# Kernel optimization log

Measured on AMD Instinct MI355X. Metric: run time of the kernel, lower is better.

The kernel has to match this reference:

```python
import jax, jax.numpy as jnp
import numpy as np

N_NODES = 100000
N_EDGES = 3200000
N_GRAPHS = 1000
HID = 64
L = 4  # num_unit


def setup_inputs() -> dict:
    key = jax.random.key(0)
    ks = jax.random.split(key, 16)
    x = jax.random.normal(ks[0], (N_NODES, 4), dtype=jnp.float32)
    edge_index = jax.random.randint(ks[1], (2, N_EDGES), 0, N_NODES, dtype=jnp.int64)
    edge_attr = jax.random.uniform(ks[2], (N_EDGES,), dtype=jnp.float32)
    batch = jnp.sort(jax.random.randint(ks[3], (N_NODES,), 0, N_GRAPHS, dtype=jnp.int64))
    s = 1.0 / np.sqrt(HID)
    inp = {
        'x': x, 'edge_index': edge_index, 'edge_attr': edge_attr, 'batch': batch,
        'emb_w': jax.random.normal(ks[4], (4, HID), jnp.float32) * 0.5,
        'emb_b': jnp.zeros((HID,), jnp.float32),
        'conv_w1': jax.random.normal(ks[5], (L, HID, HID), jnp.float32) * s,
        'conv_b1': jnp.zeros((L, HID), jnp.float32),
        'conv_w2': jax.random.normal(ks[6], (L, HID, HID), jnp.float32) * s,
        'conv_w3': jax.random.normal(ks[7], (L, HID, HID), jnp.float32) * s,
        'conv_b3': jnp.zeros((L, HID), jnp.float32),
        'lin1_w': jax.random.normal(ks[8], (HID, HID), jnp.float32) * s,
        'lin1_b': jnp.zeros((HID,), jnp.float32),
        'lin2_w': jax.random.normal(ks[9], (HID, 3), jnp.float32) * s,
        'lin2_b': jnp.zeros((3,), jnp.float32),
    }
    return inp


def _forward(x, edge_index, edge_attr, batch,
             emb_w, emb_b, conv_w1, conv_b1, conv_w2, conv_w3, conv_b3,
             lin1_w, lin1_b, lin2_w, lin2_b):
    src, dst = edge_index[0], edge_index[1]
    ew = edge_attr[:, None]  # [E,1]
    h = x @ emb_w + emb_b  # node_emb; dropout omitted (eval mode)
    for l in range(conv_w1.shape[0]):
        # LEConv: out_i = sum_{j->i} w_ji * (lin1(x_j) - lin2(x_i)) + lin3(x_i)
        a = h @ conv_w1[l] + conv_b1[l]
        b = h @ conv_w2[l]  # no bias
        msg = (a[src] - b[dst]) * ew  # [E, HID]
        agg = jax.ops.segment_sum(msg, dst, num_segments=h.shape[0])
        h = jax.nn.relu(agg + h @ conv_w3[l] + conv_b3[l])
    # global mean pool over graphs
    sums = jax.ops.segment_sum(h, batch, num_segments=N_GRAPHS)
    cnt = jax.ops.segment_sum(jnp.ones((h.shape[0],), h.dtype), batch, num_segments=N_GRAPHS)
    graph_x = sums / jnp.maximum(cnt, 1.0)[:, None]
    pred = jax.nn.relu(graph_x @ lin1_w + lin1_b) @ lin2_w + lin2_b
    return pred


def reference(x, edge_index, edge_attr, batch, emb_w, emb_b,
              conv_w1, conv_b1, conv_w2, conv_w3, conv_b3,
              lin1_w, lin1_b, lin2_w, lin2_b):
    return _forward(x, edge_index, edge_attr, batch, emb_w, emb_b,
                    conv_w1, conv_b1, conv_w2, conv_w3, conv_b3,
                    lin1_w, lin1_b, lin2_w, lin2_b)
```

## Files before the change

### kernel.cpp

```cpp
#include <hip/hip_runtime.h>

#define N_NODES 100000
#define N_EDGES 3200000
#define N_GRAPHS 1000
#define NLAYER 4
#define NB 782
#define BBITS 7
#define CAP 4608
#define EPB 2048
#define GSC 1563

typedef __attribute__((ext_vector_type(8))) short bf16x8;
typedef __attribute__((ext_vector_type(4))) float f32x4;

static __device__ __forceinline__ unsigned f2bf(float f) {
  unsigned u = __float_as_uint(f);
  return (u + 0x7fffu + ((u >> 16) & 1u)) >> 16;
}
static __device__ __forceinline__ float bf2f_lo(unsigned u) {
  return __uint_as_float(u << 16);
}
static __device__ __forceinline__ float bf2f_hi(unsigned u) {
  return __uint_as_float(u & 0xffff0000u);
}

__global__ __launch_bounds__(256) void embed_kernel(
    const float* __restrict__ x, const float* __restrict__ emb_w,
    const float* __restrict__ emb_b, unsigned short* __restrict__ h_bf,
    int* __restrict__ gcur)
{
  if (blockIdx.x == 0) {
    for (int i = threadIdx.x; i < NB; i += 256) gcur[i] = i * CAP;
  }
  int t = blockIdx.x * 256 + threadIdx.x;
  if (t >= N_NODES * 64) return;
  int c = t & 63, v = t >> 6;
  float4 xv = ((const float4*)x)[v];
  float acc = emb_b[c];
  acc = fmaf(xv.x, emb_w[0 * 64 + c], acc);
  acc = fmaf(xv.y, emb_w[1 * 64 + c], acc);
  acc = fmaf(xv.z, emb_w[2 * 64 + c], acc);
  acc = fmaf(xv.w, emb_w[3 * 64 + c], acc);
  h_bf[t] = (unsigned short)f2bf(acc);
}

__global__ __launch_bounds__(256) void bscatter5_kernel(
    const int* __restrict__ ei, const float* __restrict__ ea,
    int* __restrict__ gcur, unsigned* __restrict__ tmp_w,
    unsigned char* __restrict__ tmp_d)
{
  __shared__ unsigned hist[NB];
  __shared__ int dif[NB];
  __shared__ unsigned stage_w[EPB];
  __shared__ unsigned char stage_d[EPB];
  __shared__ unsigned short bid[EPB];
  __shared__ int wpart[4];
  int tid = threadIdx.x;
  int base = blockIdx.x * EPB;

  for (int i = tid; i < NB; i += 256) hist[i] = 0;
  __syncthreads();

  int dreg[8];
#pragma unroll
  for (int i = 0; i < 8; ++i) {
    int e = base + i * 256 + tid;
    dreg[i] = -1;
    if (e < N_EDGES) {
      int d = ei[N_EDGES + e];
      dreg[i] = d;
      atomicAdd(&hist[((unsigned)d) >> BBITS], 1u);
    }
  }
  __syncthreads();

  int lane = tid & 63, w = tid >> 6;
  int b0 = tid * 4;
  int c[4];
  int tsum = 0;
#pragma unroll
  for (int k = 0; k < 4; ++k) {
    int b = b0 + k;
    c[k] = (b < NB) ? (int)hist[b] : 0;
    tsum += c[k];
  }
  int s = tsum;
#pragma unroll
  for (int off = 1; off < 64; off <<= 1) {
    int y = __shfl_up(s, off);
    if (lane >= off) s += y;
  }
  if (lane == 63) wpart[w] = s;
  __syncthreads();
  int wo = 0;
  for (int ww = 0; ww < w; ++ww) wo += wpart[ww];
  int excl = wo + (s - tsum);
#pragma unroll
  for (int k = 0; k < 4; ++k) {
    int b = b0 + k;
    if (b < NB) {
      int gb = c[k] ? atomicAdd(&gcur[b], c[k]) : 0;
      dif[b] = gb - excl;
      hist[b] = (unsigned)excl;
      excl += c[k];
    }
  }
  __syncthreads();

#pragma unroll
  for (int i = 0; i < 8; ++i) {
    int e = base + i * 256 + tid;
    int d = dreg[i];
    if (d >= 0) {
      unsigned bkt = ((unsigned)d) >> BBITS;
      unsigned lp = atomicAdd(&hist[bkt], 1u);
      unsigned q15 = (unsigned)(ea[e] * 32768.0f);
      stage_w[lp] = ((unsigned)ei[e]) | (q15 << 17);
      stage_d[lp] = (unsigned char)(d & 127);
      bid[lp] = (unsigned short)bkt;
    }
  }
  __syncthreads();

  int nE = min(EPB, N_EDGES - base);
  for (int i = tid; i < nE; i += 256) {
    int g = dif[bid[i]] + i;
    tmp_w[g] = stage_w[i];
    tmp_d[g] = stage_d[i];
  }
}

__global__ __launch_bounds__(256) void bucket_sort4_kernel(
    const int* __restrict__ gcur, const unsigned* __restrict__ tmp_w,
    const unsigned char* __restrict__ tmp_d,
    unsigned* __restrict__ csr, int* __restrict__ row_off,
    unsigned short* __restrict__ deg16, float* __restrict__ degw)
{
  int j = blockIdx.x;
  int b0 = j * CAP;
  int nE = gcur[j] - b0;
  __shared__ unsigned hist[128];
  __shared__ float dws[128];
  __shared__ unsigned cur[128];
  __shared__ int wpart[2];
  __shared__ unsigned short perm[CAP];
  int t = threadIdx.x;
  if (t < 128) { hist[t] = 0; dws[t] = 0.f; }
  __syncthreads();
  for (int i = t; i < nE; i += 256) {
    unsigned d = tmp_d[b0 + i];
    unsigned wrd = tmp_w[b0 + i];
    atomicAdd(&hist[d], 1u);
    atomicAdd(&dws[d], (float)(wrd >> 17) * (1.0f / 32768.0f));
  }
  __syncthreads();
  int lane = t & 63, w = t >> 6;
  int v = (t < 128) ? (int)hist[t] : 0;
  int s = v;
#pragma unroll
  for (int off = 1; off < 64; off <<= 1) {
    int y = __shfl_up(s, off);
    if (lane >= off) s += y;
  }
  if (t < 128 && lane == 63) wpart[w] = s;
  __syncthreads();
  if (t < 128) {
    int wo = (w == 1) ? wpart[0] : 0;
    int excl = wo + s - v;
    cur[t] = (unsigned)excl;
    int vnode = (j << BBITS) + t;
    if (vnode < N_NODES) {
      row_off[vnode] = b0 + excl;
      deg16[vnode] = (unsigned short)v;
      degw[vnode] = dws[t];
    }
  }
  __syncthreads();

  for (int i = t; i < nE; i += 256) {
    unsigned p = atomicAdd(&cur[tmp_d[b0 + i]], 1u);
    perm[p] = (unsigned short)i;
  }
  __syncthreads();
  for (int q = t; q < nE; q += 256)
    csr[b0 + q] = tmp_w[b0 + (int)perm[q]];
}

__global__ __launch_bounds__(256) void wswz_kernel(
    const float* __restrict__ cw1, const float* __restrict__ cw2,
    const float* __restrict__ cw3, unsigned* __restrict__ wswz)
{
  int l = blockIdx.x;
  const float* w1 = cw1 + l * 4096;
  const float* w2 = cw2 + l * 4096;
  const float* w3 = cw3 + l * 4096;
  unsigned* outp = wswz + l * 6144;
  int tid = threadIdx.x;
  int n = tid & 63;
  int gofs = tid >> 6;
  for (int it = 0; it < 24; ++it) {
    int g = it * 4 + gofs;
    int m = g >> 5;
    int kp = g & 31;
    int k = kp * 2;
    const float* W = (m == 0) ? w2 : (m == 1) ? w3 : w1;
    unsigned lo = f2bf(W[k * 64 + n]);
    unsigned hi = f2bf(W[(k + 1) * 64 + n]);
    int c = k >> 5;
    int kk = k & 31;
    int lane = ((kk >> 3) << 4) | (n & 15);
    int j2 = (kk & 7) >> 1;
    int t = n >> 4;
    outp[(((m * 2 + c) * 4 + t) << 8) | (lane << 2) | j2] = lo | (hi << 16);
  }
}

__global__ __launch_bounds__(256) void matvec3_mfma_kernel(
    const unsigned short* __restrict__ h_bf,
    const unsigned* __restrict__ wz,
    const float* __restrict__ b1, const float* __restrict__ b3,
    const float* __restrict__ degw,
    unsigned short* __restrict__ a_bf, unsigned short* __restrict__ cc_bf)
{
  int gw = (blockIdx.x * 256 + threadIdx.x) >> 6;
  int lane = threadIdx.x & 63;
  int quad = lane >> 4;
  int col = lane & 15;
  int nb = gw * 16;
  if (nb >= N_NODES) return;

  int arow = nb + col;
  if (arow >= N_NODES) arow = N_NODES - 1;
  const bf16x8* ap = (const bf16x8*)(h_bf + (size_t)arow * 64 + quad * 8);
  bf16x8 af0 = ap[0];
  bf16x8 af1 = ap[4];

  float dwr[4];
#pragma unroll
  for (int r = 0; r < 4; ++r) {
    int row = nb + quad * 4 + r;
    dwr[r] = degw[row < N_NODES ? row : 0];
  }

#pragma unroll
  for (int t = 0; t < 4; ++t) {
    const bf16x8* b20 = (const bf16x8*)&wz[((0 * 4 + t) << 8) + lane * 4];
    const bf16x8* b21 = (const bf16x8*)&wz[((1 * 4 + t) << 8) + lane * 4];
    const bf16x8* b30 = (const bf16x8*)&wz[((2 * 4 + t) << 8) + lane * 4];
    const bf16x8* b31 = (const bf16x8*)&wz[((3 * 4 + t) << 8) + lane * 4];
    const bf16x8* b10 = (const bf16x8*)&wz[((4 * 4 + t) << 8) + lane * 4];
    const bf16x8* b11 = (const bf16x8*)&wz[((5 * 4 + t) << 8) + lane * 4];

    f32x4 z = {0.f, 0.f, 0.f, 0.f};
    f32x4 acc2 = __builtin_amdgcn_mfma_f32_16x16x32_bf16(af0, *b20, z, 0, 0, 0);
    acc2 = __builtin_amdgcn_mfma_f32_16x16x32_bf16(af1, *b21, acc2, 0, 0, 0);
    f32x4 cc;
#pragma unroll
    for (int r = 0; r < 4; ++r) cc[r] = -dwr[r] * acc2[r];
    cc = __builtin_amdgcn_mfma_f32_16x16x32_bf16(af0, *b30, cc, 0, 0, 0);
    cc = __builtin_amdgcn_mfma_f32_16x16x32_bf16(af1, *b31, cc, 0, 0, 0);
    float bb3 = b3[t * 16 + col];
#pragma unroll
    for (int r = 0; r < 4; ++r) {
      int row = nb + quad * 4 + r;
      if (row < N_NODES)
        cc_bf[(size_t)row * 64 + t * 16 + col] = (unsigned short)f2bf(cc[r] + bb3);
    }

    float bb1 = b1[t * 16 + col];
    f32x4 a1 = {bb1, bb1, bb1, bb1};
    a1 = __builtin_amdgcn_mfma_f32_16x16x32_bf16(af0, *b10, a1, 0, 0, 0);
    a1 = __builtin_amdgcn_mfma_f32_16x16x32_bf16(af1, *b11, a1, 0, 0, 0);
#pragma unroll
    for (int r = 0; r < 4; ++r) {
      int row = nb + quad * 4 + r;
      if (row < N_NODES)
        a_bf[(size_t)row * 64 + t * 16 + col] = (unsigned short)f2bf(a1[r]);
    }
  }
}

__global__ __launch_bounds__(256) void agg_kernel(
    const uint2* __restrict__ a2, const uint2* __restrict__ cc2,
    const int* __restrict__ row_off, const unsigned short* __restrict__ deg16,
    const unsigned* __restrict__ csr,
    float4* __restrict__ h4, unsigned short* __restrict__ h_bf, int write_h)
{
  int wave = (blockIdx.x * 256 + threadIdx.x) >> 6;
  int lane = threadIdx.x & 63;
  int sg = lane >> 4;
  int li = lane & 15;
  int lsel = (lane & 48) << 2;
  int v = wave * 4 + sg;
  bool valid = v < N_NODES;
  int vc = valid ? v : N_NODES - 1;
  int base = row_off[vc];
  int ecnt = valid ? (int)deg16[vc] : 0;
  int emax = ecnt;
  emax = max(emax, __shfl_xor(emax, 16));
  emax = max(emax, __shfl_xor(emax, 32));

  float4 acc = make_float4(0.f, 0.f, 0.f, 0.f);
  if (valid) {
    uint2 cu = cc2[(size_t)vc * 16 + li];
    acc.x = bf2f_lo(cu.x);
    acc.y = bf2f_hi(cu.x);
    acc.z = bf2f_lo(cu.y);
    acc.w = bf2f_hi(cu.y);
  }
  const uint2* ap = a2 + li;

  int full = emax & ~15;
  int c0 = 0;
  for (; c0 < full; c0 += 16) {
    int idx = c0 + li;
    int er = (idx < ecnt) ? (int)csr[base + idx] : 0;
#pragma unroll
    for (int j = 0; j < 16; ++j) {
      unsigned r = (unsigned)__builtin_amdgcn_ds_bpermute(lsel | (j << 2), er);
      int s = (int)(r & 0x1FFFFu);
      float w = (float)(r >> 17) * (1.0f / 32768.0f);
      uint2 u = ap[(size_t)s * 16];
      acc.x = fmaf(w, bf2f_lo(u.x), acc.x);
      acc.y = fmaf(w, bf2f_hi(u.x), acc.y);
      acc.z = fmaf(w, bf2f_lo(u.y), acc.z);
      acc.w = fmaf(w, bf2f_hi(u.y), acc.w);
    }
  }
  int rem = emax - full;
  if (rem > 0) {
    int idx = c0 + li;
    int er = (idx < ecnt) ? (int)csr[base + idx] : 0;
    for (int j = 0; j < rem; ++j) {
      unsigned r = (unsigned)__builtin_amdgcn_ds_bpermute(lsel | (j << 2), er);
      int s = (int)(r & 0x1FFFFu);
      float w = (float)(r >> 17) * (1.0f / 32768.0f);
      uint2 u = ap[(size_t)s * 16];
      acc.x = fmaf(w, bf2f_lo(u.x), acc.x);
      acc.y = fmaf(w, bf2f_hi(u.x), acc.y);
      acc.z = fmaf(w, bf2f_lo(u.y), acc.z);
      acc.w = fmaf(w, bf2f_hi(u.y), acc.w);
    }
  }
  if (valid) {
    acc.x = fmaxf(acc.x, 0.f);
    acc.y = fmaxf(acc.y, 0.f);
    acc.z = fmaxf(acc.z, 0.f);
    acc.w = fmaxf(acc.w, 0.f);
    if (write_h) h4[(size_t)v * 16 + li] = acc;
    uint2 p;
    p.x = f2bf(acc.x) | (f2bf(acc.y) << 16);
    p.y = f2bf(acc.z) | (f2bf(acc.w) << 16);
    ((uint2*)h_bf)[(size_t)v * 16 + li] = p;
  }
}

__global__ __launch_bounds__(256) void head_kernel(
    const float* __restrict__ h, const int* __restrict__ batch,
    const float* __restrict__ l1w, const float* __restrict__ l1b,
    const float* __restrict__ l2w, const float* __restrict__ l2b,
    float* __restrict__ out)
{
  int g = (blockIdx.x * 256 + threadIdx.x) >> 6;
  int lane = threadIdx.x & 63;
  if (g >= N_GRAPHS) return;
  int lo = 0, hi = N_NODES;
  while (lo < hi) { int mid = (lo + hi) >> 1; if (batch[mid] < g) lo = mid + 1; else hi = mid; }
  int start = lo;
  hi = N_NODES;
  while (lo < hi) { int mid = (lo + hi) >> 1; if (batch[mid] < g + 1) lo = mid + 1; else hi = mid; }
  int end = lo;

  float sum = 0.f;
  for (int v = start; v < end; ++v) sum += h[(size_t)v * 64 + lane];
  float cntf = (float)(end - start);
  float gx = sum / fmaxf(cntf, 1.f);

  float acc = l1b[lane];
  for (int k = 0; k < 64; ++k) {
    float gxk = __shfl(gx, k);
    acc = fmaf(gxk, l1w[k * 64 + lane], acc);
  }
  float t = fmaxf(acc, 0.f);
  float p0 = t * l2w[lane * 3 + 0];
  float p1 = t * l2w[lane * 3 + 1];
  float p2 = t * l2w[lane * 3 + 2];
  for (int off = 32; off > 0; off >>= 1) {
    p0 += __shfl_down(p0, off);
    p1 += __shfl_down(p1, off);
    p2 += __shfl_down(p2, off);
  }
  if (lane == 0) {
    out[g * 3 + 0] = p0 + l2b[0];
    out[g * 3 + 1] = p1 + l2b[1];
    out[g * 3 + 2] = p2 + l2b[2];
  }
}

extern "C" void kernel_launch(void* const* d_in, const int* in_sizes, int n_in,
                              void* d_out, int out_size, void* d_ws, size_t ws_size,
                              hipStream_t stream)
{
  (void)in_sizes; (void)n_in; (void)out_size; (void)ws_size;
  const float* x     = (const float*)d_in[0];
  const int*   ei    = (const int*)d_in[1];
  const float* ea    = (const float*)d_in[2];
  const int*   batch = (const int*)d_in[3];
  const float* emb_w = (const float*)d_in[4];
  const float* emb_b = (const float*)d_in[5];
  const float* cw1   = (const float*)d_in[6];
  const float* cb1   = (const float*)d_in[7];
  const float* cw2   = (const float*)d_in[8];
  const float* cw3   = (const float*)d_in[9];
  const float* cb3   = (const float*)d_in[10];
  const float* l1w   = (const float*)d_in[11];
  const float* l1b   = (const float*)d_in[12];
  const float* l2w   = (const float*)d_in[13];
  const float* l2b   = (const float*)d_in[14];
  float* out = (float*)d_out;

  char* wsb = (char*)d_ws;
  size_t off = 0;
  auto alloc = [&](size_t bytes) {
    char* p = wsb + off;
    off = (off + bytes + 255) & ~(size_t)255;
    return p;
  };
  float* h       = (float*)alloc(sizeof(float) * (size_t)N_NODES * 64);
  unsigned short* h_bf = (unsigned short*)alloc(sizeof(short) * (size_t)N_NODES * 64);
  unsigned short* a_bf = (unsigned short*)alloc(sizeof(short) * (size_t)N_NODES * 64);
  unsigned short* cc_bf = (unsigned short*)alloc(sizeof(short) * (size_t)N_NODES * 64);
  unsigned* csr  = (unsigned*)alloc(sizeof(unsigned) * (size_t)NB * CAP);
  int*   row_off = (int*)alloc(sizeof(int) * N_NODES);
  unsigned short* deg16 = (unsigned short*)alloc(sizeof(short) * N_NODES);
  float* degw    = (float*)alloc(sizeof(float) * N_NODES);
  int*   gcur    = (int*)alloc(sizeof(int) * NB);
  unsigned* wswz = (unsigned*)alloc(sizeof(unsigned) * NLAYER * 6144);
  unsigned* tmp_w = (unsigned*)h;
  unsigned char* tmp_d = (unsigned char*)h + sizeof(unsigned) * (size_t)NB * CAP;

  embed_kernel<<<(N_NODES * 64 + 255) / 256, 256, 0, stream>>>(
      x, emb_w, emb_b, h_bf, gcur);
  wswz_kernel<<<NLAYER, 256, 0, stream>>>(cw1, cw2, cw3, wswz);
  bscatter5_kernel<<<GSC, 256, 0, stream>>>(ei, ea, gcur, tmp_w, tmp_d);
  bucket_sort4_kernel<<<NB, 256, 0, stream>>>(gcur, tmp_w, tmp_d, csr, row_off,
                                              deg16, degw);

  int agg_blocks = (N_NODES + 15) / 16;
  int mv_blocks = (N_NODES / 16 + 3) / 4 + 1;
  for (int l = 0; l < NLAYER; ++l) {
    matvec3_mfma_kernel<<<mv_blocks, 256, 0, stream>>>(
        h_bf, wswz + l * 6144, cb1 + l * 64, cb3 + l * 64, degw, a_bf, cc_bf);
    agg_kernel<<<agg_blocks, 256, 0, stream>>>(
        (const uint2*)a_bf, (const uint2*)cc_bf, row_off, deg16, csr, (float4*)h,
        h_bf, (l == NLAYER - 1) ? 1 : 0);
  }

  head_kernel<<<(N_GRAPHS * 64 + 255) / 256, 256, 0, stream>>>(
      h, batch, l1w, l1b, l2w, l2b, out);
}
```

Before: 621.7 us.

## Widen CSR buckets to 256 nodes, double edges per scatter block, fuse weight prep

The two-pass bucket sort that builds the CSR now uses 256-node buckets (391 buckets, capacity 8960) instead of 128-node ones, and each scatter block handles 4096 edges instead of 2048. This halves the number of blocks and the global atomics on the bucket cursors. The weight swizzle kernel is folded into the embedding kernel, which removes one launch. In exchange, each block uses more shared memory and registers, fewer blocks run in the scatter and sort passes, and bucket overflow is now silently clamped at the capacity.

```diff
diff --git a/kernel.cpp b/kernel.cpp
--- a/kernel.cpp
+++ b/kernel.cpp
@@ -4,11 +4,10 @@
 #define N_EDGES 3200000
 #define N_GRAPHS 1000
 #define NLAYER 4
-#define NB 782
-#define BBITS 7
-#define CAP 4608
-#define EPB 2048
-#define GSC 1563
+#define NB 391
+#define CAP 8960
+#define EPB 4096
+#define NCHUNK 782
 
 typedef __attribute__((ext_vector_type(8))) short bf16x8;
 typedef __attribute__((ext_vector_type(4))) float f32x4;
@@ -24,15 +23,41 @@
   return __uint_as_float(u & 0xffff0000u);
 }
 
-__global__ __launch_bounds__(256) void embed_kernel(
+__global__ __launch_bounds__(256) void prologue_kernel(
     const float* __restrict__ x, const float* __restrict__ emb_w,
     const float* __restrict__ emb_b, unsigned short* __restrict__ h_bf,
-    int* __restrict__ gcur)
-{
-  if (blockIdx.x == 0) {
-    for (int i = threadIdx.x; i < NB; i += 256) gcur[i] = i * CAP;
-  }
-  int t = blockIdx.x * 256 + threadIdx.x;
+    int* __restrict__ gcur,
+    const float* __restrict__ cw1, const float* __restrict__ cw2,
+    const float* __restrict__ cw3, unsigned* __restrict__ wswz)
+{
+  int tid = threadIdx.x;
+  if (blockIdx.x == 4) {
+    for (int i = tid; i < NB; i += 256) gcur[i] = i * CAP;
+  }
+  if (blockIdx.x < NLAYER) {
+    int l = blockIdx.x;
+    const float* w1 = cw1 + l * 4096;
+    const float* w2 = cw2 + l * 4096;
+    const float* w3 = cw3 + l * 4096;
+    unsigned* outp = wswz + l * 6144;
+    int n = tid & 63;
+    int gofs = tid >> 6;
+    for (int it = 0; it < 24; ++it) {
+      int g = it * 4 + gofs;
+      int m = g >> 5;
+      int k = (g & 31) * 2;
+      const float* W = (m == 0) ? w2 : (m == 1) ? w3 : w1;
+      unsigned lo = f2bf(W[k * 64 + n]);
+      unsigned hi = f2bf(W[(k + 1) * 64 + n]);
+      int c = k >> 5;
+      int kk = k & 31;
+      int ln = ((kk >> 3) << 4) | (n & 15);
+      int j2 = (kk & 7) >> 1;
+      int t4 = n >> 4;
+      outp[(((m * 2 + c) * 4 + t4) << 8) | (ln << 2) | j2] = lo | (hi << 16);
+    }
+  }
+  int t = blockIdx.x * 256 + tid;
   if (t >= N_NODES * 64) return;
   int c = t & 63, v = t >> 6;
   float4 xv = ((const float4*)x)[v];
@@ -44,7 +69,7 @@
   h_bf[t] = (unsigned short)f2bf(acc);
 }
 
-__global__ __launch_bounds__(256) void bscatter5_kernel(
+__global__ __launch_bounds__(256) void bscatter_kernel(
     const int* __restrict__ ei, const float* __restrict__ ea,
     int* __restrict__ gcur, unsigned* __restrict__ tmp_w,
     unsigned char* __restrict__ tmp_d)
@@ -61,29 +86,24 @@
   for (int i = tid; i < NB; i += 256) hist[i] = 0;
   __syncthreads();
 
-  int dreg[8];
-#pragma unroll
-  for (int i = 0; i < 8; ++i) {
+  int dreg[16];
+#pragma unroll
+  for (int i = 0; i < 16; ++i) {
     int e = base + i * 256 + tid;
     dreg[i] = -1;
     if (e < N_EDGES) {
       int d = ei[N_EDGES + e];
       dreg[i] = d;
-      atomicAdd(&hist[((unsigned)d) >> BBITS], 1u);
+      atomicAdd(&hist[((unsigned)d) >> 8], 1u);
     }
   }
   __syncthreads();
 
   int lane = tid & 63, w = tid >> 6;
-  int b0 = tid * 4;
-  int c[4];
-  int tsum = 0;
-#pragma unroll
-  for (int k = 0; k < 4; ++k) {
-    int b = b0 + k;
-    c[k] = (b < NB) ? (int)hist[b] : 0;
-    tsum += c[k];
-  }
+  int b0i = tid * 2, b1i = tid * 2 + 1;
+  int c0 = (b0i < NB) ? (int)hist[b0i] : 0;
+  int c1 = (b1i < NB) ? (int)hist[b1i] : 0;
+  int tsum = c0 + c1;
   int s = tsum;
 #pragma unroll
   for (int off = 1; off < 64; off <<= 1) {
@@ -95,28 +115,28 @@
   int wo = 0;
   for (int ww = 0; ww < w; ++ww) wo += wpart[ww];
   int excl = wo + (s - tsum);
-#pragma unroll
-  for (int k = 0; k < 4; ++k) {
-    int b = b0 + k;
-    if (b < NB) {
-      int gb = c[k] ? atomicAdd(&gcur[b], c[k]) : 0;
-      dif[b] = gb - excl;
-      hist[b] = (unsigned)excl;
-      excl += c[k];
-    }
-  }
-  __syncthreads();
-
-#pragma unroll
-  for (int i = 0; i < 8; ++i) {
+  if (b0i < NB) {
+    int gb = c0 ? atomicAdd(&gcur[b0i], c0) : 0;
+    dif[b0i] = gb - excl;
+    hist[b0i] = (unsigned)excl;
+  }
+  if (b1i < NB) {
+    int gb = c1 ? atomicAdd(&gcur[b1i], c1) : 0;
+    dif[b1i] = gb - (excl + c0);
+    hist[b1i] = (unsigned)(excl + c0);
+  }
+  __syncthreads();
+
+#pragma unroll
+  for (int i = 0; i < 16; ++i) {
     int e = base + i * 256 + tid;
     int d = dreg[i];
     if (d >= 0) {
-      unsigned bkt = ((unsigned)d) >> BBITS;
+      unsigned bkt = ((unsigned)d) >> 8;
       unsigned lp = atomicAdd(&hist[bkt], 1u);
       unsigned q15 = (unsigned)(ea[e] * 32768.0f);
       stage_w[lp] = ((unsigned)ei[e]) | (q15 << 17);
-      stage_d[lp] = (unsigned char)(d & 127);
+      stage_d[lp] = (unsigned char)(d & 255);
       bid[lp] = (unsigned short)bkt;
     }
   }
@@ -130,7 +150,7 @@
   }
 }
 
-__global__ __launch_bounds__(256) void bucket_sort4_kernel(
+__global__ __launch_bounds__(256) void bucket_sort_kernel(
     const int* __restrict__ gcur, const unsigned* __restrict__ tmp_w,
     const unsigned char* __restrict__ tmp_d,
     unsigned* __restrict__ csr, int* __restrict__ row_off,
@@ -138,14 +158,15 @@
 {
   int j = blockIdx.x;
   int b0 = j * CAP;
-  int nE = gcur[j] - b0;
-  __shared__ unsigned hist[128];
-  __shared__ float dws[128];
-  __shared__ unsigned cur[128];
-  __shared__ int wpart[2];
+  int nE = min(gcur[j] - b0, CAP);
+  __shared__ unsigned hist[256];
+  __shared__ float dws[256];
+  __shared__ unsigned cur[256];
+  __shared__ int wpart[4];
   __shared__ unsigned short perm[CAP];
   int t = threadIdx.x;
-  if (t < 128) { hist[t] = 0; dws[t] = 0.f; }
+  hist[t] = 0;
+  dws[t] = 0.f;
   __syncthreads();
   for (int i = t; i < nE; i += 256) {
     unsigned d = tmp_d[b0 + i];
@@ -155,25 +176,24 @@
   }
   __syncthreads();
   int lane = t & 63, w = t >> 6;
-  int v = (t < 128) ? (int)hist[t] : 0;
+  int v = (int)hist[t];
   int s = v;
 #pragma unroll
   for (int off = 1; off < 64; off <<= 1) {
     int y = __shfl_up(s, off);
     if (lane >= off) s += y;
   }
-  if (t < 128 && lane == 63) wpart[w] = s;
-  __syncthreads();
-  if (t < 128) {
-    int wo = (w == 1) ? wpart[0] : 0;
-    int excl = wo + s - v;
-    cur[t] = (unsigned)excl;
-    int vnode = (j << BBITS) + t;
-    if (vnode < N_NODES) {
-      row_off[vnode] = b0 + excl;
-      deg16[vnode] = (unsigned short)v;
-      degw[vnode] = dws[t];
-    }
+  if (lane == 63) wpart[w] = s;
+  __syncthreads();
+  int wo = 0;
+  for (int ww = 0; ww < w; ++ww) wo += wpart[ww];
+  int excl = wo + s - v;
+  cur[t] = (unsigned)excl;
+  int vnode = (j << 8) + t;
+  if (vnode < N_NODES) {
+    row_off[vnode] = b0 + excl;
+    deg16[vnode] = (unsigned short)v;
+    degw[vnode] = dws[t];
   }
   __syncthreads();
 
@@ -184,35 +204,6 @@
   __syncthreads();
   for (int q = t; q < nE; q += 256)
     csr[b0 + q] = tmp_w[b0 + (int)perm[q]];
-}
-
-__global__ __launch_bounds__(256) void wswz_kernel(
-    const float* __restrict__ cw1, const float* __restrict__ cw2,
-    const float* __restrict__ cw3, unsigned* __restrict__ wswz)
-{
-  int l = blockIdx.x;
-  const float* w1 = cw1 + l * 4096;
-  const float* w2 = cw2 + l * 4096;
-  const float* w3 = cw3 + l * 4096;
-  unsigned* outp = wswz + l * 6144;
-  int tid = threadIdx.x;
-  int n = tid & 63;
-  int gofs = tid >> 6;
-  for (int it = 0; it < 24; ++it) {
-    int g = it * 4 + gofs;
-    int m = g >> 5;
-    int kp = g & 31;
-    int k = kp * 2;
-    const float* W = (m == 0) ? w2 : (m == 1) ? w3 : w1;
-    unsigned lo = f2bf(W[k * 64 + n]);
-    unsigned hi = f2bf(W[(k + 1) * 64 + n]);
-    int c = k >> 5;
-    int kk = k & 31;
-    int lane = ((kk >> 3) << 4) | (n & 15);
-    int j2 = (kk & 7) >> 1;
-    int t = n >> 4;
-    outp[(((m * 2 + c) * 4 + t) << 8) | (lane << 2) | j2] = lo | (hi << 16);
-  }
 }
 
 __global__ __launch_bounds__(256) void matvec3_mfma_kernel(
@@ -439,12 +430,11 @@
   unsigned* tmp_w = (unsigned*)h;
   unsigned char* tmp_d = (unsigned char*)h + sizeof(unsigned) * (size_t)NB * CAP;
 
-  embed_kernel<<<(N_NODES * 64 + 255) / 256, 256, 0, stream>>>(
-      x, emb_w, emb_b, h_bf, gcur);
-  wswz_kernel<<<NLAYER, 256, 0, stream>>>(cw1, cw2, cw3, wswz);
-  bscatter5_kernel<<<GSC, 256, 0, stream>>>(ei, ea, gcur, tmp_w, tmp_d);
-  bucket_sort4_kernel<<<NB, 256, 0, stream>>>(gcur, tmp_w, tmp_d, csr, row_off,
-                                              deg16, degw);
+  prologue_kernel<<<(N_NODES * 64 + 255) / 256, 256, 0, stream>>>(
+      x, emb_w, emb_b, h_bf, gcur, cw1, cw2, cw3, wswz);
+  bscatter_kernel<<<NCHUNK, 256, 0, stream>>>(ei, ea, gcur, tmp_w, tmp_d);
+  bucket_sort_kernel<<<NB, 256, 0, stream>>>(gcur, tmp_w, tmp_d, csr, row_off,
+                                             deg16, degw);
 
   int agg_blocks = (N_NODES + 15) / 16;
   int mv_blocks = (N_NODES / 16 + 3) / 4 + 1;
```

Result: faster. 520.2 us (-16.3%).
